# Optimization experiments

Measured on AMD Instinct MI355X. Metric: run time of the kernel, lower is better.

The kernel has to match this reference:

```python
import jax, jax.numpy as jnp
import numpy as np


def _spectral_normalize(W):
    # spectral_norm divides the weight by its largest singular value
    sigma = jnp.linalg.norm(W, ord=2)
    return W / sigma


def setup_inputs() -> dict:
    key = jax.random.key(0)
    ks = jax.random.split(key, 8)
    B, C, H, W = 2, 64, 96, 96
    C8 = C // 8
    x = jax.random.normal(ks[0], (B, C, H, W), dtype=jnp.float32)
    Wq = jax.random.normal(ks[1], (C8, C), dtype=jnp.float32) * 0.1
    bq = jax.random.normal(ks[2], (C8,), dtype=jnp.float32) * 0.1
    Wk = jax.random.normal(ks[3], (C8, C), dtype=jnp.float32) * 0.1
    bk = jax.random.normal(ks[4], (C8,), dtype=jnp.float32) * 0.1
    Wv = jax.random.normal(ks[5], (C, C), dtype=jnp.float32) * 0.1
    bv = jax.random.normal(ks[6], (C,), dtype=jnp.float32) * 0.1
    gamma = jnp.ones((1,), dtype=jnp.float32)
    return {"x": x, "Wq": Wq, "bq": bq, "Wk": Wk, "bk": bk,
            "Wv": Wv, "bv": bv, "gamma": gamma}


def reference(x, Wq, bq, Wk, bk, Wv, bv, gamma):
    B, C, H, W = x.shape
    xf = x.reshape(B, C, H * W)                       # [B, C, N]
    Wq_n = _spectral_normalize(Wq)
    Wk_n = _spectral_normalize(Wk)
    Wv_n = _spectral_normalize(Wv)
    # 1x1 Conv1d == matmul over channel dim
    f = jnp.einsum('oc,bcn->bon', Wq_n, xf) + bq[None, :, None]   # [B, C/8, N]
    g = jnp.einsum('oc,bcn->bon', Wk_n, xf) + bk[None, :, None]   # [B, C/8, N]
    h = jnp.einsum('oc,bcn->bon', Wv_n, xf) + bv[None, :, None]   # [B, C, N]
    # scores[b,i,j] = sum_c f[b,c,i] * g[b,c,j];  softmax over dim=1 (i)
    scores = jnp.einsum('bci,bcj->bij', f, g)                      # [B, N, N]
    beta = jax.nn.softmax(scores, axis=1)
    # o[b,c,j] = sum_i h[b,c,i] * beta[b,i,j]
    o = gamma[0] * jnp.einsum('bci,bij->bcj', h, beta) + xf
    return o.reshape(B, C, H, W)
```

## Files before the change

kernel.cpp:

```cpp
#include <hip/hip_runtime.h>


#define N_PIX 9216
#define N_B   2
#define N_C   64

typedef _Float16 half8  __attribute__((ext_vector_type(8)));
typedef _Float16 half4v __attribute__((ext_vector_type(4)));
typedef float    float4v __attribute__((ext_vector_type(4)));
typedef int      int4v  __attribute__((ext_vector_type(4)));

#define LOG2E 1.44269504088896340736f
#define EXP_SHIFT 12.0f

__global__ __launch_bounds__(64) void k_sigma(const float* __restrict__ Wq,
                                              const float* __restrict__ Wk,
                                              const float* __restrict__ Wv,
                                              float* __restrict__ sig) {
  __shared__ float G8[8][8];
  __shared__ float Wl[64 * 64];
  __shared__ _Float16 Wh[64 * 80];
  __shared__ _Float16 Gh[64 * 80];
  const int t = threadIdx.x;
  const int mat = blockIdx.x;
  if (mat < 2) {
    const float* W = (mat == 0) ? Wq : Wk;
    const int i = t >> 3, j = t & 7;
    float g = 0.f;
    for (int c = 0; c < 64; ++c) g += W[i * 64 + c] * W[j * 64 + c];
    G8[i][j] = g;
    __syncthreads();
    const int L = t & 7;
    float G0[8], Gr[8];
    for (int k = 0; k < 8; ++k) { G0[k] = G8[L][k]; Gr[k] = G0[k]; }
    for (int it = 0; it < 8; ++it) {
      float g2[8] = {0, 0, 0, 0, 0, 0, 0, 0};
      for (int k = 0; k < 8; ++k) {
        float gik = Gr[k];
        for (int jj = 0; jj < 8; ++jj) g2[jj] += gik * __shfl(Gr[jj], k, 64);
      }
      float mx = 0.f;
      for (int jj = 0; jj < 8; ++jj) mx = fmaxf(mx, fabsf(g2[jj]));
      for (int d = 1; d < 8; d <<= 1) mx = fmaxf(mx, __shfl_xor(mx, d, 64));
      float r = 1.f / mx;
      for (int jj = 0; jj < 8; ++jj) Gr[jj] = g2[jj] * r;
    }
    float u = 0.f;
    for (int jj = 0; jj < 8; ++jj) u += Gr[jj];
    float y = 0.f;
    for (int k = 0; k < 8; ++k) y += G0[k] * __shfl(u, k, 64);
    float nu = u * y, de = u * u;
    for (int d = 1; d < 8; d <<= 1) { nu += __shfl_xor(nu, d, 64); de += __shfl_xor(de, d, 64); }
    if (t == 0) sig[mat] = sqrtf(nu / de);
  } else {
    for (int idx = t; idx < 4096; idx += 64) Wl[idx] = Wv[idx];
    __syncthreads();
    for (int idx = t; idx < 4096; idx += 64) Wh[(idx >> 6) * 80 + (idx & 63)] = (_Float16)Wl[idx];
    __syncthreads();
    const int lane15 = t & 15, quad = t >> 4;
    half8 fr[4][2];
    for (int rb = 0; rb < 4; ++rb)
      for (int kc = 0; kc < 2; ++kc)
        fr[rb][kc] = *(const half8*)&Wh[(lane15 + 16 * rb) * 80 + 32 * kc + 8 * quad];
    float4v D[4][4];
    for (int mb = 0; mb < 4; ++mb) for (int nb = 0; nb < 4; ++nb) D[mb][nb] = (float4v){0.f, 0.f, 0.f, 0.f};
    for (int kc = 0; kc < 2; ++kc)
      for (int mb = 0; mb < 4; ++mb)
        for (int nb = 0; nb < 4; ++nb)
          D[mb][nb] = __builtin_amdgcn_mfma_f32_16x16x32_f16(fr[mb][kc], fr[nb][kc], D[mb][nb], 0, 0, 0);
    for (int it = 0; it < 8; ++it) {
      float mx = 0.f;
      for (int mb = 0; mb < 4; ++mb) for (int nb = 0; nb < 4; ++nb) for (int r = 0; r < 4; ++r)
        mx = fmaxf(mx, fabsf(D[mb][nb][r]));
      for (int d = 1; d < 64; d <<= 1) mx = fmaxf(mx, __shfl_xor(mx, d, 64));
      float rs = 1.f / mx;
      for (int mb = 0; mb < 4; ++mb) for (int nb = 0; nb < 4; ++nb) for (int r = 0; r < 4; ++r)
        Gh[(4 * quad + r + 16 * mb) * 80 + lane15 + 16 * nb] = (_Float16)(D[mb][nb][r] * rs);
      __syncthreads();
      if (it == 7) break;
      for (int rb = 0; rb < 4; ++rb)
        for (int kc = 0; kc < 2; ++kc)
          fr[rb][kc] = *(const half8*)&Gh[(lane15 + 16 * rb) * 80 + 32 * kc + 8 * quad];
      for (int mb = 0; mb < 4; ++mb) for (int nb = 0; nb < 4; ++nb) D[mb][nb] = (float4v){0.f, 0.f, 0.f, 0.f};
      for (int kc = 0; kc < 2; ++kc)
        for (int mb = 0; mb < 4; ++mb)
          for (int nb = 0; nb < 4; ++nb)
            D[mb][nb] = __builtin_amdgcn_mfma_f32_16x16x32_f16(fr[mb][kc], fr[nb][kc], D[mb][nb], 0, 0, 0);
      __syncthreads();
    }
    float u = 0.f;
    for (int c = 0; c < 64; ++c) u += (float)Gh[t * 80 + c];
    float z = 0.f;
    for (int i2 = 0; i2 < 64; ++i2) z += Wl[i2 * 64 + t] * __shfl(u, i2, 64);
    float nu = z * z, de = u * u;
    for (int d = 1; d < 64; d <<= 1) { nu += __shfl_xor(nu, d, 64); de += __shfl_xor(de, d, 64); }
    if (t == 0) sig[2] = sqrtf(nu / de);
  }
}

__global__ __launch_bounds__(128) void k_wconv(const float* __restrict__ Wq, const float* __restrict__ bq,
                                               const float* __restrict__ Wk, const float* __restrict__ bk,
                                               const float* __restrict__ Wv, const float* __restrict__ bv,
                                               const float* __restrict__ sig,
                                               _Float16* __restrict__ W16, float* __restrict__ b80,
                                               unsigned* __restrict__ maxKu) {
  const float iq = LOG2E / sig[0], ik = 1.0f / sig[1], iv = 1.0f / sig[2];
  const int t = threadIdx.x;
  for (int idx = t; idx < 80 * 64; idx += 128) {
    const int m = idx >> 6, c = idx & 63;
    float v;
    if (m < 8)       v = Wq[m * 64 + c] * iq;
    else if (m < 16) v = Wk[(m - 8) * 64 + c] * ik;
    else             v = Wv[(m - 16) * 64 + c] * iv;
    W16[idx] = (_Float16)v;
  }
  if (t < 80) {
    float v;
    if (t < 8)       v = bq[t] * LOG2E;
    else if (t < 16) v = bk[t - 8];
    else             v = bv[t - 16];
    b80[t] = v;
  }
  if (t < 2) maxKu[t] = 0u;
}

__global__ __launch_bounds__(256) void k_fgh(const float* __restrict__ x,
                                             const _Float16* __restrict__ W16,
                                             const float* __restrict__ b80,
                                             _Float16* __restrict__ K16,
                                             _Float16* __restrict__ Q16,
                                             _Float16* __restrict__ VT16,
                                             unsigned* __restrict__ maxKu) {
  const int wave = threadIdx.x >> 6;
  const int lane = threadIdx.x & 63;
  const int lane15 = lane & 15, quad = lane >> 4;
  const int tile = blockIdx.x * 4 + wave;
  const int b = tile / 576;
  const int n = (tile % 576) * 16 + lane15;
  half8 wf[5][2];
  for (int mb = 0; mb < 5; ++mb)
    for (int kc = 0; kc < 2; ++kc)
      wf[mb][kc] = *(const half8*)&W16[(lane15 + 16 * mb) * 64 + 32 * kc + 8 * quad];
  float4v acc[5];
  for (int mb = 0; mb < 5; ++mb) acc[mb] = *(const float4v*)&b80[16 * mb + 4 * quad];
  const float* xb = x + (size_t)b * N_C * N_PIX;
  for (int kc = 0; kc < 2; ++kc) {
    half8 bf;
    for (int j = 0; j < 8; ++j)
      bf[j] = (_Float16)xb[(size_t)(32 * kc + 8 * quad + j) * N_PIX + n];
    for (int mb = 0; mb < 5; ++mb)
      acc[mb] = __builtin_amdgcn_mfma_f32_16x16x32_f16(wf[mb][kc], bf, acc[mb], 0, 0, 0);
  }
  {
    _Float16* dstK = K16 + ((size_t)b * N_PIX + n) * 8;
    _Float16* dstQ = Q16 + ((size_t)b * N_PIX + n) * 8;
    for (int r = 0; r < 4; ++r) {
      const int m = 4 * quad + r;
      const _Float16 v = (_Float16)acc[0][r];
      if (m < 8) dstK[m] = v; else dstQ[m - 8] = v;
    }
  }
  for (int mb = 1; mb < 5; ++mb)
    for (int r = 0; r < 4; ++r) {
      const int c = 4 * quad + r + 16 * (mb - 1);
      VT16[((size_t)b * N_C + c) * N_PIX + n] = (_Float16)acc[mb][r];
    }
  float sq = 0.f;
  if (quad < 2)
    for (int r = 0; r < 4; ++r) sq += acc[0][r] * acc[0][r];
  sq += __shfl_xor(sq, 16, 64);
  for (int d = 1; d < 64; d <<= 1) sq = fmaxf(sq, __shfl_xor(sq, d, 64));
  if (lane == 0) atomicMax(&maxKu[b], __float_as_uint(sq));
}


__device__ __forceinline__ void gload16(const _Float16* g, _Float16* l) {
  __builtin_amdgcn_global_load_lds(
      (const __attribute__((address_space(1))) void*)g,
      (__attribute__((address_space(3))) void*)l, 16, 0, 0);
}

#define VMWAIT5() asm volatile("s_waitcnt vmcnt(5)" ::: "memory")
#define DS2(D0, D1, P0, P1)                                              \
  asm volatile("ds_read_b128 %0, %2\n\t"                                 \
               "ds_read_b128 %1, %3\n\t"                                 \
               "s_waitcnt lgkmcnt(0)"                                    \
               : "=&v"(D0), "=&v"(D1) : "v"(P0), "v"(P1) : "memory")
#define DS4(D0, D1, D2, D3, P0, P1, P2, P3)                              \
  asm volatile("ds_read_b128 %0, %4\n\t"                                 \
               "ds_read_b128 %1, %5\n\t"                                 \
               "ds_read_b128 %2, %6\n\t"                                 \
               "ds_read_b128 %3, %7\n\t"                                 \
               "s_waitcnt lgkmcnt(0)"                                    \
               : "=&v"(D0), "=&v"(D1), "=&v"(D2), "=&v"(D3)              \
               : "v"(P0), "v"(P1), "v"(P2), "v"(P3) : "memory")
typedef const __attribute__((address_space(3))) _Float16* lds_cp;

__global__ __launch_bounds__(256, 2) void k_attn(const _Float16* __restrict__ K16,
                                                 const _Float16* __restrict__ Q16,
                                                 const _Float16* __restrict__ VT16,
                                                 const unsigned* __restrict__ maxKu,
                                                 const float* __restrict__ x,
                                                 const float* __restrict__ gamma,
                                                 float* __restrict__ out) {
  __shared__ __align__(16) _Float16 Kld[2][4][64 * 8];
  __shared__ __align__(16) _Float16 Vld[2][4][64 * 32];
  __shared__ __align__(16) _Float16 Pld[4][32 * 40];
  __shared__ float Lsh[4][32];
  __shared__ float Osh[4][64][17];
  const int wave = threadIdx.x >> 6;
  const int lane = threadIdx.x & 63;
  const int lane15 = lane & 15, quad = lane >> 4;
  const int tile = blockIdx.x;
  const int b = tile / 288;
  const int jb = (tile % 288) * 32;
  const float gm = gamma[0];
  const _Float16* Kb = K16 + (size_t)b * N_PIX * 8;
  const _Float16* Vb = VT16 + (size_t)b * N_C * N_PIX;
  _Float16* Pl = Pld[wave];

  half8 qf0 = {}, qf1 = {};
  if (quad == 0) {
    qf0 = *(const half8*)(Q16 + ((size_t)b * N_PIX + jb + lane15) * 8);
    qf1 = *(const half8*)(Q16 + ((size_t)b * N_PIX + jb + 16 + lane15) * 8);
  }
  const float maxK = sqrtf(__uint_as_float(maxKu[b]));
  float nq0 = 0.f, nq1 = 0.f;
  if (quad == 0)
#pragma unroll
    for (int j = 0; j < 8; ++j) {
      nq0 += (float)qf0[j] * (float)qf0[j];
      nq1 += (float)qf1[j] * (float)qf1[j];
    }
  nq0 = __shfl(nq0, lane15, 64);
  nq1 = __shfl(nq1, lane15, 64);
  const float M0 = sqrtf(nq0) * maxK - EXP_SHIFT;
  const float M1 = sqrtf(nq1) * maxK - EXP_SHIFT;

  float4v a00 = {0.f,0.f,0.f,0.f}, a01 = {0.f,0.f,0.f,0.f}, a02 = {0.f,0.f,0.f,0.f}, a03 = {0.f,0.f,0.f,0.f};
  float4v a10 = {0.f,0.f,0.f,0.f}, a11 = {0.f,0.f,0.f,0.f}, a12 = {0.f,0.f,0.f,0.f}, a13 = {0.f,0.f,0.f,0.f};
  float ls0 = 0.f, ls1 = 0.f;
  const float4v f4z = {0.f, 0.f, 0.f, 0.f};

#define STAGE(SLOT, I0)                                                          \
  {                                                                              \
    const int _i = (I0);                                                         \
    gload16(Kb + (size_t)(_i + (lane & 31)) * 8, &Kld[SLOT][wave][0]);           \
    gload16(Vb + (size_t)(lane >> 2) * N_PIX + _i + (lane & 3) * 8,              \
            &Vld[SLOT][wave][0]);                                                \
    gload16(Vb + (size_t)(16 + (lane >> 2)) * N_PIX + _i + (lane & 3) * 8,       \
            &Vld[SLOT][wave][512]);                                              \
    gload16(Vb + (size_t)(32 + (lane >> 2)) * N_PIX + _i + (lane & 3) * 8,       \
            &Vld[SLOT][wave][1024]);                                             \
    gload16(Vb + (size_t)(48 + (lane >> 2)) * N_PIX + _i + (lane & 3) * 8,       \
            &Vld[SLOT][wave][1536]);                                             \
  }

  STAGE(0, 32 * wave)

#pragma unroll 1
  for (int r = 0; r < 72; ++r) {
    const int slot = r & 1, nslot = slot ^ 1;
    const int i1 = (r < 71) ? (128 * (r + 1) + 32 * wave) : (128 * 71 + 32 * wave);
    STAGE(nslot, i1)
    VMWAIT5();
    int4v k0i, k1i;
    {
      lds_cp pk0 = (lds_cp)&Kld[slot][wave][lane15 * 8];
      lds_cp pk1 = (lds_cp)&Kld[slot][wave][(16 + lane15) * 8];
      DS2(k0i, k1i, pk0, pk1);
    }
    const half8 kf0 = __builtin_bit_cast(half8, k0i);
    const half8 kf1 = __builtin_bit_cast(half8, k1i);
    float4v s00 = __builtin_amdgcn_mfma_f32_16x16x32_f16(kf0, qf0, f4z, 0, 0, 0);
    float4v s10 = __builtin_amdgcn_mfma_f32_16x16x32_f16(kf1, qf0, f4z, 0, 0, 0);
    float4v s01 = __builtin_amdgcn_mfma_f32_16x16x32_f16(kf0, qf1, f4z, 0, 0, 0);
    float4v s11 = __builtin_amdgcn_mfma_f32_16x16x32_f16(kf1, qf1, f4z, 0, 0, 0);
    half4v h00, h10, h01, h11;
#pragma unroll
    for (int rr = 0; rr < 4; ++rr) {
      const float p00 = __builtin_amdgcn_exp2f(s00[rr] - M0);
      const float p10 = __builtin_amdgcn_exp2f(s10[rr] - M0);
      const float p01 = __builtin_amdgcn_exp2f(s01[rr] - M1);
      const float p11 = __builtin_amdgcn_exp2f(s11[rr] - M1);
      h00[rr] = (_Float16)p00; ls0 += (float)h00[rr];
      h10[rr] = (_Float16)p10; ls0 += (float)h10[rr];
      h01[rr] = (_Float16)p01; ls1 += (float)h01[rr];
      h11[rr] = (_Float16)p11; ls1 += (float)h11[rr];
    }
    *(half4v*)&Pl[lane15 * 40 + 4 * quad] = h00;
    *(half4v*)&Pl[lane15 * 40 + 16 + 4 * quad] = h10;
    *(half4v*)&Pl[(16 + lane15) * 40 + 4 * quad] = h01;
    *(half4v*)&Pl[(16 + lane15) * 40 + 16 + 4 * quad] = h11;
    const half8 pf0 = *(const half8*)&Pl[lane15 * 40 + 8 * quad];
    const half8 pf1 = *(const half8*)&Pl[(16 + lane15) * 40 + 8 * quad];
    int4v v0i, v1i, v2i, v3i;
    {
      lds_cp pv0 = (lds_cp)&Vld[slot][wave][lane15 * 32 + 8 * quad];
      lds_cp pv1 = (lds_cp)&Vld[slot][wave][512 + lane15 * 32 + 8 * quad];
      lds_cp pv2 = (lds_cp)&Vld[slot][wave][1024 + lane15 * 32 + 8 * quad];
      lds_cp pv3 = (lds_cp)&Vld[slot][wave][1536 + lane15 * 32 + 8 * quad];
      DS4(v0i, v1i, v2i, v3i, pv0, pv1, pv2, pv3);
    }
    a00 = __builtin_amdgcn_mfma_f32_16x16x32_f16(pf0, __builtin_bit_cast(half8, v0i), a00, 0, 0, 0);
    a01 = __builtin_amdgcn_mfma_f32_16x16x32_f16(pf0, __builtin_bit_cast(half8, v1i), a01, 0, 0, 0);
    a02 = __builtin_amdgcn_mfma_f32_16x16x32_f16(pf0, __builtin_bit_cast(half8, v2i), a02, 0, 0, 0);
    a03 = __builtin_amdgcn_mfma_f32_16x16x32_f16(pf0, __builtin_bit_cast(half8, v3i), a03, 0, 0, 0);
    a10 = __builtin_amdgcn_mfma_f32_16x16x32_f16(pf1, __builtin_bit_cast(half8, v0i), a10, 0, 0, 0);
    a11 = __builtin_amdgcn_mfma_f32_16x16x32_f16(pf1, __builtin_bit_cast(half8, v1i), a11, 0, 0, 0);
    a12 = __builtin_amdgcn_mfma_f32_16x16x32_f16(pf1, __builtin_bit_cast(half8, v2i), a12, 0, 0, 0);
    a13 = __builtin_amdgcn_mfma_f32_16x16x32_f16(pf1, __builtin_bit_cast(half8, v3i), a13, 0, 0, 0);
  }
#undef STAGE
  asm volatile("s_waitcnt vmcnt(0)" ::: "memory");

  ls0 += __shfl_xor(ls0, 16, 64); ls0 += __shfl_xor(ls0, 32, 64);
  ls1 += __shfl_xor(ls1, 16, 64); ls1 += __shfl_xor(ls1, 32, 64);
  if (quad == 0) { Lsh[wave][lane15] = ls0; Lsh[wave][16 + lane15] = ls1; }
#pragma unroll
  for (int rr = 0; rr < 4; ++rr) {
    Osh[wave][lane][rr]      = a00[rr];
    Osh[wave][lane][4 + rr]  = a01[rr];
    Osh[wave][lane][8 + rr]  = a02[rr];
    Osh[wave][lane][12 + rr] = a03[rr];
  }
  __syncthreads();
  float4v lt0 = {0.f, 0.f, 0.f, 0.f}, lt1 = {0.f, 0.f, 0.f, 0.f};
#pragma unroll
  for (int w = 0; w < 4; ++w) {
    const float4v a = *(const float4v*)&Lsh[w][4 * quad];
    const float4v c = *(const float4v*)&Lsh[w][16 + 4 * quad];
#pragma unroll
    for (int rr = 0; rr < 4; ++rr) { lt0[rr] += a[rr]; lt1[rr] += c[rr]; }
  }
  const int ch = 16 * wave + lane15;
  const float* xb = x + (size_t)b * N_C * N_PIX;
  float* ob = out + (size_t)b * N_C * N_PIX;
  {
    float4v osum = {0.f, 0.f, 0.f, 0.f};
#pragma unroll
    for (int w = 0; w < 4; ++w)
#pragma unroll
      for (int rr = 0; rr < 4; ++rr) osum[rr] += Osh[w][lane][4 * wave + rr];
    const size_t idx = (size_t)ch * N_PIX + jb + 4 * quad;
    const float4v xr = *(const float4v*)(xb + idx);
    float4v o;
#pragma unroll
    for (int rr = 0; rr < 4; ++rr) o[rr] = gm * osum[rr] / lt0[rr] + xr[rr];
    *(float4v*)(ob + idx) = o;
  }
  __syncthreads();
#pragma unroll
  for (int rr = 0; rr < 4; ++rr) {
    Osh[wave][lane][rr]      = a10[rr];
    Osh[wave][lane][4 + rr]  = a11[rr];
    Osh[wave][lane][8 + rr]  = a12[rr];
    Osh[wave][lane][12 + rr] = a13[rr];
  }
  __syncthreads();
  {
    float4v osum = {0.f, 0.f, 0.f, 0.f};
#pragma unroll
    for (int w = 0; w < 4; ++w)
#pragma unroll
      for (int rr = 0; rr < 4; ++rr) osum[rr] += Osh[w][lane][4 * wave + rr];
    const size_t idx = (size_t)ch * N_PIX + jb + 16 + 4 * quad;
    const float4v xr = *(const float4v*)(xb + idx);
    float4v o;
#pragma unroll
    for (int rr = 0; rr < 4; ++rr) o[rr] = gm * osum[rr] / lt1[rr] + xr[rr];
    *(float4v*)(ob + idx) = o;
  }
}

extern "C" void kernel_launch(void* const* d_in, const int* in_sizes, int n_in,
                              void* d_out, int out_size, void* d_ws, size_t ws_size,
                              hipStream_t stream) {
  const float* x     = (const float*)d_in[0];
  const float* Wq    = (const float*)d_in[1];
  const float* bq    = (const float*)d_in[2];
  const float* Wk    = (const float*)d_in[3];
  const float* bk    = (const float*)d_in[4];
  const float* Wv    = (const float*)d_in[5];
  const float* bv    = (const float*)d_in[6];
  const float* gamma = (const float*)d_in[7];
  float* out = (float*)d_out;

  char* ws = (char*)d_ws;
  float*    sig   = (float*)ws;
  unsigned* maxKu = (unsigned*)(ws + 16);
  float*    b80   = (float*)(ws + 32);
  _Float16* W16   = (_Float16*)(ws + 512);
  _Float16* K16   = (_Float16*)(ws + 10752);
  _Float16* Q16   = (_Float16*)(ws + 10752 + 294912);
  _Float16* VT16  = (_Float16*)(ws + 10752 + 2 * 294912);

  hipLaunchKernelGGL(k_sigma, dim3(3), dim3(64), 0, stream, Wq, Wk, Wv, sig);
  hipLaunchKernelGGL(k_wconv, dim3(1), dim3(128), 0, stream, Wq, bq, Wk, bk, Wv, bv, sig, W16, b80, maxKu);
  hipLaunchKernelGGL(k_fgh, dim3(288), dim3(256), 0, stream, x, W16, b80, K16, Q16, VT16, maxKu);
  hipLaunchKernelGGL(k_attn, dim3(576), dim3(256), 0, stream, K16, Q16, VT16, maxKu, x, gamma, out);
}
```

Baseline: 198.0 us.

## Fuse weight conversion into projection kernel and compact attention LDS for occupancy

Removes the single-block k_wconv launch: each k_fgh block now scales and converts the weights and biases into shared memory itself, and k_sigma zeroes maxKu. In k_attn, the separate K/V/P/O/L shared buffers are merged into one per-wave region that is reused for the epilogue. The V layout is XOR-swizzled to reduce bank conflicts, and launch bounds are raised to 3 blocks per CU. This cuts one launch and one serial dependency, and the smaller LDS footprint allows higher occupancy. The cost is redundant weight conversion in every block, plus register pressure from the tighter launch bound.

```diff
diff --git a/kernel.cpp b/kernel.cpp
--- a/kernel.cpp
+++ b/kernel.cpp
@@ -16,13 +16,15 @@
 __global__ __launch_bounds__(64) void k_sigma(const float* __restrict__ Wq,
                                               const float* __restrict__ Wk,
                                               const float* __restrict__ Wv,
-                                              float* __restrict__ sig) {
+                                              float* __restrict__ sig,
+                                              unsigned* __restrict__ maxKu) {
   __shared__ float G8[8][8];
   __shared__ float Wl[64 * 64];
   __shared__ _Float16 Wh[64 * 80];
   __shared__ _Float16 Gh[64 * 80];
   const int t = threadIdx.x;
   const int mat = blockIdx.x;
+  if (mat == 0 && t < 2) maxKu[t] = 0u;
   if (mat < 2) {
     const float* W = (mat == 0) ? Wq : Wk;
     const int i = t >> 3, j = t & 7;
@@ -98,41 +100,37 @@
   }
 }
 
-__global__ __launch_bounds__(128) void k_wconv(const float* __restrict__ Wq, const float* __restrict__ bq,
-                                               const float* __restrict__ Wk, const float* __restrict__ bk,
-                                               const float* __restrict__ Wv, const float* __restrict__ bv,
-                                               const float* __restrict__ sig,
-                                               _Float16* __restrict__ W16, float* __restrict__ b80,
-                                               unsigned* __restrict__ maxKu) {
+__global__ __launch_bounds__(256) void k_fgh(const float* __restrict__ x,
+                                             const float* __restrict__ Wq, const float* __restrict__ bq,
+                                             const float* __restrict__ Wk, const float* __restrict__ bk,
+                                             const float* __restrict__ Wv, const float* __restrict__ bv,
+                                             const float* __restrict__ sig,
+                                             _Float16* __restrict__ K16,
+                                             _Float16* __restrict__ Q16,
+                                             _Float16* __restrict__ VT16,
+                                             unsigned* __restrict__ maxKu) {
+  __shared__ _Float16 Wsh[80 * 64];
+  __shared__ float bsh[80];
+  const int t = threadIdx.x;
   const float iq = LOG2E / sig[0], ik = 1.0f / sig[1], iv = 1.0f / sig[2];
-  const int t = threadIdx.x;
-  for (int idx = t; idx < 80 * 64; idx += 128) {
+  for (int idx = t; idx < 80 * 64; idx += 256) {
     const int m = idx >> 6, c = idx & 63;
     float v;
     if (m < 8)       v = Wq[m * 64 + c] * iq;
     else if (m < 16) v = Wk[(m - 8) * 64 + c] * ik;
     else             v = Wv[(m - 16) * 64 + c] * iv;
-    W16[idx] = (_Float16)v;
+    Wsh[idx] = (_Float16)v;
   }
   if (t < 80) {
     float v;
     if (t < 8)       v = bq[t] * LOG2E;
     else if (t < 16) v = bk[t - 8];
     else             v = bv[t - 16];
-    b80[t] = v;
-  }
-  if (t < 2) maxKu[t] = 0u;
-}
-
-__global__ __launch_bounds__(256) void k_fgh(const float* __restrict__ x,
-                                             const _Float16* __restrict__ W16,
-                                             const float* __restrict__ b80,
-                                             _Float16* __restrict__ K16,
-                                             _Float16* __restrict__ Q16,
-                                             _Float16* __restrict__ VT16,
-                                             unsigned* __restrict__ maxKu) {
-  const int wave = threadIdx.x >> 6;
-  const int lane = threadIdx.x & 63;
+    bsh[t] = v;
+  }
+  __syncthreads();
+  const int wave = t >> 6;
+  const int lane = t & 63;
   const int lane15 = lane & 15, quad = lane >> 4;
   const int tile = blockIdx.x * 4 + wave;
   const int b = tile / 576;
@@ -140,9 +138,9 @@
   half8 wf[5][2];
   for (int mb = 0; mb < 5; ++mb)
     for (int kc = 0; kc < 2; ++kc)
-      wf[mb][kc] = *(const half8*)&W16[(lane15 + 16 * mb) * 64 + 32 * kc + 8 * quad];
+      wf[mb][kc] = *(const half8*)&Wsh[(lane15 + 16 * mb) * 64 + 32 * kc + 8 * quad];
   float4v acc[5];
-  for (int mb = 0; mb < 5; ++mb) acc[mb] = *(const float4v*)&b80[16 * mb + 4 * quad];
+  for (int mb = 0; mb < 5; ++mb) acc[mb] = *(const float4v*)&bsh[16 * mb + 4 * quad];
   const float* xb = x + (size_t)b * N_C * N_PIX;
   for (int kc = 0; kc < 2; ++kc) {
     half8 bf;
@@ -196,18 +194,14 @@
                : "v"(P0), "v"(P1), "v"(P2), "v"(P3) : "memory")
 typedef const __attribute__((address_space(3))) _Float16* lds_cp;
 
-__global__ __launch_bounds__(256, 2) void k_attn(const _Float16* __restrict__ K16,
+__global__ __launch_bounds__(256, 3) void k_attn(const _Float16* __restrict__ K16,
                                                  const _Float16* __restrict__ Q16,
                                                  const _Float16* __restrict__ VT16,
                                                  const unsigned* __restrict__ maxKu,
                                                  const float* __restrict__ x,
                                                  const float* __restrict__ gamma,
                                                  float* __restrict__ out) {
-  __shared__ __align__(16) _Float16 Kld[2][4][64 * 8];
-  __shared__ __align__(16) _Float16 Vld[2][4][64 * 32];
-  __shared__ __align__(16) _Float16 Pld[4][32 * 40];
-  __shared__ float Lsh[4][32];
-  __shared__ float Osh[4][64][17];
+  __shared__ __align__(16) _Float16 SM[4][6400];
   const int wave = threadIdx.x >> 6;
   const int lane = threadIdx.x & 63;
   const int lane15 = lane & 15, quad = lane >> 4;
@@ -217,7 +211,12 @@
   const float gm = gamma[0];
   const _Float16* Kb = K16 + (size_t)b * N_PIX * 8;
   const _Float16* Vb = VT16 + (size_t)b * N_C * N_PIX;
-  _Float16* Pl = Pld[wave];
+  _Float16* Rg = SM[wave];
+  _Float16* Pl = Rg + 5120;
+  const int cl = lane >> 2, kk = lane & 3;
+  const int gsw = (kk ^ ((cl >> 1) & 3)) * 8;
+  const int ksrc = lane & 31;
+  const int vslot = (quad ^ ((lane15 >> 1) & 3)) * 8;
 
   half8 qf0 = {}, qf1 = {};
   if (quad == 0) {
@@ -245,15 +244,11 @@
 #define STAGE(SLOT, I0)                                                          \
   {                                                                              \
     const int _i = (I0);                                                         \
-    gload16(Kb + (size_t)(_i + (lane & 31)) * 8, &Kld[SLOT][wave][0]);           \
-    gload16(Vb + (size_t)(lane >> 2) * N_PIX + _i + (lane & 3) * 8,              \
-            &Vld[SLOT][wave][0]);                                                \
-    gload16(Vb + (size_t)(16 + (lane >> 2)) * N_PIX + _i + (lane & 3) * 8,       \
-            &Vld[SLOT][wave][512]);                                              \
-    gload16(Vb + (size_t)(32 + (lane >> 2)) * N_PIX + _i + (lane & 3) * 8,       \
-            &Vld[SLOT][wave][1024]);                                             \
-    gload16(Vb + (size_t)(48 + (lane >> 2)) * N_PIX + _i + (lane & 3) * 8,       \
-            &Vld[SLOT][wave][1536]);                                             \
+    gload16(Kb + (size_t)(_i + ksrc) * 8, Rg + 4096 + (SLOT) * 512);             \
+    gload16(Vb + (size_t)cl * N_PIX + _i + gsw,        Rg + (SLOT) * 2048);      \
+    gload16(Vb + (size_t)(16 + cl) * N_PIX + _i + gsw, Rg + (SLOT) * 2048 + 512);\
+    gload16(Vb + (size_t)(32 + cl) * N_PIX + _i + gsw, Rg + (SLOT) * 2048 + 1024);\
+    gload16(Vb + (size_t)(48 + cl) * N_PIX + _i + gsw, Rg + (SLOT) * 2048 + 1536);\
   }
 
   STAGE(0, 32 * wave)
@@ -266,8 +261,8 @@
     VMWAIT5();
     int4v k0i, k1i;
     {
-      lds_cp pk0 = (lds_cp)&Kld[slot][wave][lane15 * 8];
-      lds_cp pk1 = (lds_cp)&Kld[slot][wave][(16 + lane15) * 8];
+      lds_cp pk0 = (lds_cp)(Rg + 4096 + slot * 512 + lane15 * 8);
+      lds_cp pk1 = (lds_cp)(Rg + 4096 + slot * 512 + 128 + lane15 * 8);
       DS2(k0i, k1i, pk0, pk1);
     }
     const half8 kf0 = __builtin_bit_cast(half8, k0i);
@@ -296,10 +291,10 @@
     const half8 pf1 = *(const half8*)&Pl[(16 + lane15) * 40 + 8 * quad];
     int4v v0i, v1i, v2i, v3i;
     {
-      lds_cp pv0 = (lds_cp)&Vld[slot][wave][lane15 * 32 + 8 * quad];
-      lds_cp pv1 = (lds_cp)&Vld[slot][wave][512 + lane15 * 32 + 8 * quad];
-      lds_cp pv2 = (lds_cp)&Vld[slot][wave][1024 + lane15 * 32 + 8 * quad];
-      lds_cp pv3 = (lds_cp)&Vld[slot][wave][1536 + lane15 * 32 + 8 * quad];
+      lds_cp pv0 = (lds_cp)(Rg + slot * 2048 + lane15 * 32 + vslot);
+      lds_cp pv1 = (lds_cp)(Rg + slot * 2048 + 512 + lane15 * 32 + vslot);
+      lds_cp pv2 = (lds_cp)(Rg + slot * 2048 + 1024 + lane15 * 32 + vslot);
+      lds_cp pv3 = (lds_cp)(Rg + slot * 2048 + 1536 + lane15 * 32 + vslot);
       DS4(v0i, v1i, v2i, v3i, pv0, pv1, pv2, pv3);
     }
     a00 = __builtin_amdgcn_mfma_f32_16x16x32_f16(pf0, __builtin_bit_cast(half8, v0i), a00, 0, 0, 0);
@@ -314,24 +309,28 @@
 #undef STAGE
   asm volatile("s_waitcnt vmcnt(0)" ::: "memory");
 
+  float* Ow = (float*)Rg;
+  float* Lw = (float*)Rg + 1088;
   ls0 += __shfl_xor(ls0, 16, 64); ls0 += __shfl_xor(ls0, 32, 64);
   ls1 += __shfl_xor(ls1, 16, 64); ls1 += __shfl_xor(ls1, 32, 64);
-  if (quad == 0) { Lsh[wave][lane15] = ls0; Lsh[wave][16 + lane15] = ls1; }
+  if (quad == 0) { Lw[lane15] = ls0; Lw[16 + lane15] = ls1; }
 #pragma unroll
   for (int rr = 0; rr < 4; ++rr) {
-    Osh[wave][lane][rr]      = a00[rr];
-    Osh[wave][lane][4 + rr]  = a01[rr];
-    Osh[wave][lane][8 + rr]  = a02[rr];
-    Osh[wave][lane][12 + rr] = a03[rr];
+    Ow[lane * 17 + rr]      = a00[rr];
+    Ow[lane * 17 + 4 + rr]  = a01[rr];
+    Ow[lane * 17 + 8 + rr]  = a02[rr];
+    Ow[lane * 17 + 12 + rr] = a03[rr];
   }
   __syncthreads();
   float4v lt0 = {0.f, 0.f, 0.f, 0.f}, lt1 = {0.f, 0.f, 0.f, 0.f};
 #pragma unroll
   for (int w = 0; w < 4; ++w) {
-    const float4v a = *(const float4v*)&Lsh[w][4 * quad];
-    const float4v c = *(const float4v*)&Lsh[w][16 + 4 * quad];
-#pragma unroll
-    for (int rr = 0; rr < 4; ++rr) { lt0[rr] += a[rr]; lt1[rr] += c[rr]; }
+    const float* Lww = (const float*)SM[w] + 1088;
+#pragma unroll
+    for (int rr = 0; rr < 4; ++rr) {
+      lt0[rr] += Lww[4 * quad + rr];
+      lt1[rr] += Lww[16 + 4 * quad + rr];
+    }
   }
   const int ch = 16 * wave + lane15;
   const float* xb = x + (size_t)b * N_C * N_PIX;
@@ -339,9 +338,11 @@
   {
     float4v osum = {0.f, 0.f, 0.f, 0.f};
 #pragma unroll
-    for (int w = 0; w < 4; ++w)
-#pragma unroll
-      for (int rr = 0; rr < 4; ++rr) osum[rr] += Osh[w][lane][4 * wave + rr];
+    for (int w = 0; w < 4; ++w) {
+      const float* Oww = (const float*)SM[w];
+#pragma unroll
+      for (int rr = 0; rr < 4; ++rr) osum[rr] += Oww[lane * 17 + 4 * wave + rr];
+    }
     const size_t idx = (size_t)ch * N_PIX + jb + 4 * quad;
     const float4v xr = *(const float4v*)(xb + idx);
     float4v o;
@@ -352,18 +353,20 @@
   __syncthreads();
 #pragma unroll
   for (int rr = 0; rr < 4; ++rr) {
-    Osh[wave][lane][rr]      = a10[rr];
-    Osh[wave][lane][4 + rr]  = a11[rr];
-    Osh[wave][lane][8 + rr]  = a12[rr];
-    Osh[wave][lane][12 + rr] = a13[rr];
+    Ow[lane * 17 + rr]      = a10[rr];
+    Ow[lane * 17 + 4 + rr]  = a11[rr];
+    Ow[lane * 17 + 8 + rr]  = a12[rr];
+    Ow[lane * 17 + 12 + rr] = a13[rr];
   }
   __syncthreads();
   {
     float4v osum = {0.f, 0.f, 0.f, 0.f};
 #pragma unroll
-    for (int w = 0; w < 4; ++w)
-#pragma unroll
-      for (int rr = 0; rr < 4; ++rr) osum[rr] += Osh[w][lane][4 * wave + rr];
+    for (int w = 0; w < 4; ++w) {
+      const float* Oww = (const float*)SM[w];
+#pragma unroll
+      for (int rr = 0; rr < 4; ++rr) osum[rr] += Oww[lane * 17 + 4 * wave + rr];
+    }
     const size_t idx = (size_t)ch * N_PIX + jb + 16 + 4 * quad;
     const float4v xr = *(const float4v*)(xb + idx);
     float4v o;
@@ -389,14 +392,12 @@
   char* ws = (char*)d_ws;
   float*    sig   = (float*)ws;
   unsigned* maxKu = (unsigned*)(ws + 16);
-  float*    b80   = (float*)(ws + 32);
-  _Float16* W16   = (_Float16*)(ws + 512);
   _Float16* K16   = (_Float16*)(ws + 10752);
   _Float16* Q16   = (_Float16*)(ws + 10752 + 294912);
   _Float16* VT16  = (_Float16*)(ws + 10752 + 2 * 294912);
 
-  hipLaunchKernelGGL(k_sigma, dim3(3), dim3(64), 0, stream, Wq, Wk, Wv, sig);
-  hipLaunchKernelGGL(k_wconv, dim3(1), dim3(128), 0, stream, Wq, bq, Wk, bk, Wv, bv, sig, W16, b80, maxKu);
-  hipLaunchKernelGGL(k_fgh, dim3(288), dim3(256), 0, stream, x, W16, b80, K16, Q16, VT16, maxKu);
+  hipLaunchKernelGGL(k_sigma, dim3(3), dim3(64), 0, stream, Wq, Wk, Wv, sig, maxKu);
+  hipLaunchKernelGGL(k_fgh, dim3(288), dim3(256), 0, stream,
+                     x, Wq, bq, Wk, bk, Wv, bv, sig, K16, Q16, VT16, maxKu);
   hipLaunchKernelGGL(k_attn, dim3(576), dim3(256), 0, stream, K16, Q16, VT16, maxKu, x, gamma, out);
 }
```

Measured after the change: 178.1 us. 10.1% less time.
